# Optimization experiments

Measured on AMD Instinct MI355X. Metric: run time of the kernel, lower is better.

Reference implementation:

```python
import jax, jax.numpy as jnp
import numpy as np

B = 1024        # number of molecule pairs (batch_don.max()+1)
LMAX = 160      # static pad length per molecule (avg ~64 atoms, 12-sigma safe)
D = 128         # embed_dim
H = 4           # num_heads
HD = D // H     # head_dim
SCALE = HD ** -0.5
LN_EPS = 1e-5


def setup_inputs() -> dict:
    key = jax.random.key(0)
    ks = jax.random.split(key, 16)
    N = 65536
    x_don = jax.random.normal(ks[0], (N, D), jnp.float32)
    x_acc = jax.random.normal(ks[1], (N, D), jnp.float32)
    batch_don = jnp.sort(jax.random.randint(ks[2], (N,), 0, B)).astype(jnp.int32)
    batch_acc = jnp.sort(jax.random.randint(ks[3], (N,), 0, B)).astype(jnp.int32)
    s = 1.0 / np.sqrt(D)
    Wq = jax.random.uniform(ks[4], (D, D), jnp.float32, -s, s)
    bq = jax.random.uniform(ks[5], (D,), jnp.float32, -s, s)
    Wk = jax.random.uniform(ks[6], (D, D), jnp.float32, -s, s)
    bk = jax.random.uniform(ks[7], (D,), jnp.float32, -s, s)
    Wv = jax.random.uniform(ks[8], (D, D), jnp.float32, -s, s)
    bv = jax.random.uniform(ks[9], (D,), jnp.float32, -s, s)
    Wo = jax.random.uniform(ks[10], (D, D), jnp.float32, -s, s)
    bo = jax.random.uniform(ks[11], (D,), jnp.float32, -s, s)
    ln_g = jnp.ones((D,), jnp.float32)
    ln_b = jnp.zeros((D,), jnp.float32)
    return {"x_don": x_don, "x_acc": x_acc, "Wq": Wq, "bq": bq, "Wk": Wk, "bk": bk,
            "Wv": Wv, "bv": bv, "Wo": Wo, "bo": bo, "ln_g": ln_g, "ln_b": ln_b,
            "batch_don": batch_don, "batch_acc": batch_acc}


def _pad_segments(x, batch):
    # sorted segment ids -> padded [B, LMAX, D], valid mask [B, LMAX], per-row pos
    n = x.shape[0]
    counts = jnp.zeros((B,), jnp.int32).at[batch].add(1)
    starts = jnp.concatenate([jnp.zeros((1,), jnp.int32), jnp.cumsum(counts)[:-1]])
    pos = jnp.arange(n, dtype=jnp.int32) - starts[batch]
    padded = jnp.zeros((B, LMAX, x.shape[1]), x.dtype).at[batch, pos].set(x)
    mask = jnp.arange(LMAX, dtype=jnp.int32)[None, :] < counts[:, None]
    return padded, mask, pos


def _layer_norm(x, g, b):
    mu = jnp.mean(x, axis=-1, keepdims=True)
    var = jnp.mean((x - mu) ** 2, axis=-1, keepdims=True)
    return (x - mu) * jax.lax.rsqrt(var + LN_EPS) * g + b


def _cross_attn(q_pad, kv_pad, k_mask, Wq, bq, Wk, bk, Wv, bv, Wo, bo, ln_g, ln_b):
    # q_pad: [B, Lq, D], kv_pad: [B, Lk, D], k_mask: [B, Lk]
    Q = (q_pad @ Wq + bq).reshape(B, LMAX, H, HD)
    K = (kv_pad @ Wk + bk).reshape(B, LMAX, H, HD)
    V = (kv_pad @ Wv + bv).reshape(B, LMAX, H, HD)
    scores = jnp.einsum('bqhd,bkhd->bhqk', Q, K) * SCALE
    scores = jnp.where(k_mask[:, None, None, :], scores, -1e30)
    m = jnp.max(scores, axis=-1, keepdims=True)
    e = jnp.exp(scores - m) * k_mask[:, None, None, :]
    attn = e / jnp.maximum(jnp.sum(e, axis=-1, keepdims=True), 1e-9)
    attended = jnp.einsum('bhqk,bkhd->bqhd', attn, V).reshape(B, LMAX, D)
    attended = attended @ Wo + bo
    # NOTE: the original module uses self.norm_don for BOTH directions (norm_acc unused)
    return _layer_norm(q_pad + attended, ln_g, ln_b)


def reference(x_don, x_acc, Wq, bq, Wk, bk, Wv, bv, Wo, bo, ln_g, ln_b, batch_don, batch_acc):
    don_pad, don_mask, don_pos = _pad_segments(x_don, batch_don)
    acc_pad, acc_mask, acc_pos = _pad_segments(x_acc, batch_acc)
    out_don = _cross_attn(don_pad, acc_pad, acc_mask, Wq, bq, Wk, bk, Wv, bv, Wo, bo, ln_g, ln_b)
    out_acc = _cross_attn(acc_pad, don_pad, don_mask, Wq, bq, Wk, bk, Wv, bv, Wo, bo, ln_g, ln_b)
    x_don_enriched = out_don[batch_don, don_pos]
    x_acc_enriched = out_acc[batch_acc, acc_pos]
    return (x_don_enriched, x_acc_enriched)
```

## Files before the change

kernel.cpp:

```cpp
#include <hip/hip_runtime.h>
#include <stdint.h>

#define NB 1024
#define LMAX 160
#define DIM 128
#define NH 4
#define HDIM 32
#define ATT_SCALE 0.1767766952966369f
#define LN_EPS 1e-5f
#define VTP 164
#define PSP 40
#define WTP 136

typedef __attribute__((ext_vector_type(8))) short bf16x8;
typedef __attribute__((ext_vector_type(4))) float f32x4;

union U8 { uint2 u[2]; uint4 q; bf16x8 v; };

__device__ __forceinline__ ushort f2bf(float f) {
    uint32_t x = __float_as_uint(f);
    x += 0x7fffu + ((x >> 16) & 1u);
    return (ushort)(x >> 16);
}
__device__ __forceinline__ uint32_t pk2bf(float a, float b) {
    return (uint32_t)f2bf(a) | ((uint32_t)f2bf(b) << 16);
}

__device__ __forceinline__ void wgbar_noflush() {
    asm volatile("s_waitcnt lgkmcnt(0)" ::: "memory");
    __builtin_amdgcn_s_barrier();
    asm volatile("" ::: "memory");
}

__global__ void setup_kernel(const float* __restrict__ Wq, const float* __restrict__ Wk,
                             const float* __restrict__ Wv, const float* __restrict__ Wo,
                             ushort* __restrict__ wtg,
                             const int* __restrict__ bd, const int* __restrict__ ba,
                             int* __restrict__ starts, int* __restrict__ counts, int N)
{
    int t = blockIdx.x * blockDim.x + threadIdx.x;
    {
        int m = t >> 14;
        int idx = t & 16383;
        int k = idx >> 7, c = idx & 127;
        const float* W = (m == 0) ? Wq : (m == 1) ? Wk : (m == 2) ? Wv : Wo;
        wtg[(m << 14) + c * DIM + k] = f2bf(W[idx]);
    }
    if (t < 2 * NB) {
        int side = t >> 10;
        int b = t & (NB - 1);
        const int* arr = side ? ba : bd;
        int lo = 0, hi = N;
        while (lo < hi) { int mid = (lo + hi) >> 1; if (arr[mid] < b) lo = mid + 1; else hi = mid; }
        int st = lo;
        hi = N;
        while (lo < hi) { int mid = (lo + hi) >> 1; if (arr[mid] < b + 1) lo = mid + 1; else hi = mid; }
        starts[t] = st;
        counts[t] = lo - st;
    }
}

__global__ __launch_bounds__(256) void proj_mfma(
    const float* __restrict__ x_don, const float* __restrict__ x_acc,
    const ushort* __restrict__ wtg,
    const float* __restrict__ bq, const float* __restrict__ bk, const float* __restrict__ bv,
    ushort* __restrict__ qkv, int N)
{
    __shared__ ushort wt[128][WTP];
    const int side = blockIdx.y;
    const float* x = side ? x_acc : x_don;
    const int t = threadIdx.x;
    const int lane = t & 63, wid = t >> 6;
    const int r16 = lane & 15, kg = lane >> 4;
    const int wr0 = blockIdx.x * 128 + wid * 32;

    float4 raw[2][4][2];
    #pragma unroll
    for (int rt = 0; rt < 2; ++rt) {
        const float* xr = &x[(size_t)(wr0 + rt * 16 + r16) * DIM + kg * 8];
        #pragma unroll
        for (int ks = 0; ks < 4; ++ks) {
            raw[rt][ks][0] = *reinterpret_cast<const float4*>(xr + ks * 32);
            raw[rt][ks][1] = *reinterpret_cast<const float4*>(xr + ks * 32 + 4);
        }
    }
    U8 xb[2][4];
    #pragma unroll
    for (int rt = 0; rt < 2; ++rt)
        #pragma unroll
        for (int ks = 0; ks < 4; ++ks) {
            xb[rt][ks].u[0].x = pk2bf(raw[rt][ks][0].x, raw[rt][ks][0].y);
            xb[rt][ks].u[0].y = pk2bf(raw[rt][ks][0].z, raw[rt][ks][0].w);
            xb[rt][ks].u[1].x = pk2bf(raw[rt][ks][1].x, raw[rt][ks][1].y);
            xb[rt][ks].u[1].y = pk2bf(raw[rt][ks][1].z, raw[rt][ks][1].w);
        }

    for (int w = 0; w < 3; ++w) {
        if (w) wgbar_noflush();

        const ushort* wsrc = wtg + ((size_t)w << 14);
        #pragma unroll
        for (int p = 0; p < 8; ++p) {
            int lin = (p * 256 + t) * 8;
            int c = lin >> 7, k = lin & 127;
            *reinterpret_cast<uint4*>(&wt[c][k]) =
                *reinterpret_cast<const uint4*>(&wsrc[c * DIM + k]);
        }
        wgbar_noflush();

        f32x4 acc[2][8];
        #pragma unroll
        for (int i = 0; i < 2; ++i)
            #pragma unroll
            for (int j = 0; j < 8; ++j) acc[i][j] = (f32x4){0.f, 0.f, 0.f, 0.f};

        #pragma unroll
        for (int ks = 0; ks < 4; ++ks)
            #pragma unroll
            for (int ct = 0; ct < 8; ++ct) {
                bf16x8 bfr = *reinterpret_cast<const bf16x8*>(
                    &wt[ct * 16 + r16][ks * 32 + kg * 8]);
                acc[0][ct] = __builtin_amdgcn_mfma_f32_16x16x32_bf16(xb[0][ks].v, bfr, acc[0][ct], 0, 0, 0);
                acc[1][ct] = __builtin_amdgcn_mfma_f32_16x16x32_bf16(xb[1][ks].v, bfr, acc[1][ct], 0, 0, 0);
            }

        const float* bias = (w == 0) ? bq : (w == 1) ? bk : bv;
        float b8[8];
        #pragma unroll
        for (int ct = 0; ct < 8; ++ct) b8[ct] = bias[ct * 16 + r16];
        ushort* outp = qkv + (size_t)(side * 3 + w) * N * DIM;
        #pragma unroll
        for (int rt = 0; rt < 2; ++rt)
            #pragma unroll
            for (int ct = 0; ct < 8; ++ct)
                #pragma unroll
                for (int j = 0; j < 4; ++j) {
                    int rr = wr0 + rt * 16 + kg * 4 + j;
                    outp[(size_t)rr * DIM + ct * 16 + r16] = f2bf(acc[rt][ct][j] + b8[ct]);
                }
    }
}

__global__ __launch_bounds__(64, 4) void attn_mfma(
    ushort* __restrict__ qkv,
    const int* __restrict__ starts, const int* __restrict__ counts, int N)
{
    __shared__ __align__(16) ushort Vt[HDIM][VTP];
    __shared__ __align__(16) ushort Ps[16][PSP];
    const int b = blockIdx.x, dir = blockIdx.y;
    const int hcol = blockIdx.z * HDIM;
    const int qside = dir, kside = 1 - dir;
    const int qs = starts[qside * NB + b];
    const int nq = counts[qside * NB + b];
    if (nq == 0) return;
    const int kst = starts[kside * NB + b];
    const int nk = min(counts[kside * NB + b], LMAX);
    ushort* Q = qkv + (size_t)(qside * 3) * N * DIM;
    const ushort* K = qkv + (size_t)(kside * 3 + 1) * N * DIM;
    const ushort* V = qkv + (size_t)(kside * 3 + 2) * N * DIM;
    const int lane = threadIdx.x;
    const int r16 = lane & 15, g = lane >> 4;

    const int NCK = (nk + 31) >> 5;
    const int NKP = NCK << 5;

    {
        const int krl = lane >> 2, c = lane & 3;
        for (int base = 0; base < nk; base += 16) {
            int kr = base + krl;
            if (kr < nk) {
                uint4 v4 = *reinterpret_cast<const uint4*>(
                    &V[(size_t)(kst + kr) * DIM + hcol + c * 8]);
                uint32_t vv[4] = {v4.x, v4.y, v4.z, v4.w};
                #pragma unroll
                for (int m2 = 0; m2 < 4; ++m2) {
                    Vt[c * 8 + 2 * m2][kr]     = (ushort)(vv[m2] & 0xffffu);
                    Vt[c * 8 + 2 * m2 + 1][kr] = (ushort)(vv[m2] >> 16);
                }
            }
        }
        int pad = NKP - nk;
        for (int i = lane; i < (pad << 5); i += 64) {
            int d = i & 31, col = nk + (i >> 5);
            Vt[d][col] = 0;
        }
    }
    __syncthreads();

    for (int q0 = 0; q0 < nq; q0 += 16) {
        const int rq = qs + min(q0 + r16, nq - 1);
        bf16x8 bQ = *reinterpret_cast<const bf16x8*>(&Q[(size_t)rq * DIM + hcol + g * 8]);

        float m = -1e30f, l = 0.f;
        f32x4 oa0 = {0.f, 0.f, 0.f, 0.f}, oa1 = {0.f, 0.f, 0.f, 0.f};

        for (int ck = 0; ck < NCK; ++ck) {
            const int k0 = ck * 32;
            const int rk0 = kst + min(k0 + r16, nk - 1);
            const int rk1 = kst + min(k0 + 16 + r16, nk - 1);
            bf16x8 aK0 = *reinterpret_cast<const bf16x8*>(&K[(size_t)rk0 * DIM + hcol + g * 8]);
            bf16x8 aK1 = *reinterpret_cast<const bf16x8*>(&K[(size_t)rk1 * DIM + hcol + g * 8]);
            f32x4 s0 = __builtin_amdgcn_mfma_f32_16x16x32_bf16(
                aK0, bQ, (f32x4){0.f, 0.f, 0.f, 0.f}, 0, 0, 0);
            f32x4 s1 = __builtin_amdgcn_mfma_f32_16x16x32_bf16(
                aK1, bQ, (f32x4){0.f, 0.f, 0.f, 0.f}, 0, 0, 0);

            float sv[8];
            #pragma unroll
            for (int j = 0; j < 4; ++j) {
                sv[j]     = (k0 + 4 * g + j < nk)      ? s0[j] * ATT_SCALE : -1e30f;
                sv[4 + j] = (k0 + 16 + 4 * g + j < nk) ? s1[j] * ATT_SCALE : -1e30f;
            }
            float tm = fmaxf(fmaxf(fmaxf(sv[0], sv[1]), fmaxf(sv[2], sv[3])),
                             fmaxf(fmaxf(sv[4], sv[5]), fmaxf(sv[6], sv[7])));
            tm = fmaxf(tm, __shfl_xor(tm, 16));
            tm = fmaxf(tm, __shfl_xor(tm, 32));

            bool up = tm > m + 8.f;
            float mn = up ? tm : m;
            float corr = up ? __expf(m - tm) : 1.f;

            float e[8];
            #pragma unroll
            for (int j = 0; j < 8; ++j) e[j] = __expf(sv[j] - mn);
            float ps = ((e[0] + e[1]) + (e[2] + e[3])) + ((e[4] + e[5]) + (e[6] + e[7]));
            ps += __shfl_xor(ps, 16);
            ps += __shfl_xor(ps, 32);
            l = l * corr + ps;
            m = mn;
            #pragma unroll
            for (int j = 0; j < 4; ++j) { oa0[j] *= corr; oa1[j] *= corr; }

            uint2 w0, w1;
            w0.x = pk2bf(e[0], e[1]);
            w0.y = pk2bf(e[2], e[3]);
            w1.x = pk2bf(e[4], e[5]);
            w1.y = pk2bf(e[6], e[7]);
            *reinterpret_cast<uint2*>(&Ps[r16][4 * g]) = w0;
            *reinterpret_cast<uint2*>(&Ps[r16][16 + 4 * g]) = w1;
            bf16x8 bP = *reinterpret_cast<const bf16x8*>(&Ps[r16][g * 8]);

            U8 av0, av1;
            av0.u[0] = *reinterpret_cast<const uint2*>(&Vt[r16][k0 + g * 8]);
            av0.u[1] = *reinterpret_cast<const uint2*>(&Vt[r16][k0 + g * 8 + 4]);
            av1.u[0] = *reinterpret_cast<const uint2*>(&Vt[16 + r16][k0 + g * 8]);
            av1.u[1] = *reinterpret_cast<const uint2*>(&Vt[16 + r16][k0 + g * 8 + 4]);
            oa0 = __builtin_amdgcn_mfma_f32_16x16x32_bf16(av0.v, bP, oa0, 0, 0, 0);
            oa1 = __builtin_amdgcn_mfma_f32_16x16x32_bf16(av1.v, bP, oa1, 0, 0, 0);
        }

        if (q0 + r16 < nq) {
            float inv = 1.f / fmaxf(l, 1e-9f);
            ushort* dst = &Q[(size_t)(qs + q0 + r16) * DIM + hcol];
            uint2 o0, o1;
            o0.x = pk2bf(oa0[0] * inv, oa0[1] * inv);
            o0.y = pk2bf(oa0[2] * inv, oa0[3] * inv);
            o1.x = pk2bf(oa1[0] * inv, oa1[1] * inv);
            o1.y = pk2bf(oa1[2] * inv, oa1[3] * inv);
            *reinterpret_cast<uint2*>(dst + 4 * g) = o0;
            *reinterpret_cast<uint2*>(dst + 16 + 4 * g) = o1;
        }
    }
}

__global__ __launch_bounds__(256) void out_mfma(
    const ushort* __restrict__ qkv,
    const float* __restrict__ x_don, const float* __restrict__ x_acc,
    const ushort* __restrict__ wtg,
    const float* __restrict__ bo, const float* __restrict__ ln_g, const float* __restrict__ ln_b,
    float* __restrict__ out, int N)
{
    __shared__ ushort wt[128][WTP];
    const int t = threadIdx.x;
    const int lane = t & 63, wid = t >> 6;
    const int r16 = lane & 15, kg = lane >> 4;
    const int r0 = blockIdx.x * 128;
    const int wr0 = r0 + wid * 32;
    const ushort* attb = qkv + (r0 < N ? (size_t)0 : (size_t)2 * N * DIM);
    const float* xresb = (r0 < N) ? x_don : x_acc;
    const int rx0 = (r0 < N) ? wr0 : wr0 - N;

    const ushort* wsrc = wtg + ((size_t)3 << 14);
    #pragma unroll
    for (int p = 0; p < 8; ++p) {
        int lin = (p * 256 + t) * 8;
        int c = lin >> 7, k = lin & 127;
        *reinterpret_cast<uint4*>(&wt[c][k]) =
            *reinterpret_cast<const uint4*>(&wsrc[c * DIM + k]);
    }

    U8 ab[2][4];
    #pragma unroll
    for (int rt = 0; rt < 2; ++rt)
        #pragma unroll
        for (int ks = 0; ks < 4; ++ks)
            ab[rt][ks].q = *reinterpret_cast<const uint4*>(
                &attb[(size_t)(wr0 + rt * 16 + r16) * DIM + ks * 32 + kg * 8]);

    __syncthreads();

    f32x4 acc[2][8];
    #pragma unroll
    for (int i = 0; i < 2; ++i)
        #pragma unroll
        for (int j = 0; j < 8; ++j) acc[i][j] = (f32x4){0.f, 0.f, 0.f, 0.f};

    #pragma unroll
    for (int ks = 0; ks < 4; ++ks)
        #pragma unroll
        for (int ct = 0; ct < 8; ++ct) {
            bf16x8 bfr = *reinterpret_cast<const bf16x8*>(
                &wt[ct * 16 + r16][ks * 32 + kg * 8]);
            acc[0][ct] = __builtin_amdgcn_mfma_f32_16x16x32_bf16(ab[0][ks].v, bfr, acc[0][ct], 0, 0, 0);
            acc[1][ct] = __builtin_amdgcn_mfma_f32_16x16x32_bf16(ab[1][ks].v, bfr, acc[1][ct], 0, 0, 0);
        }

    float bo8[8], g8[8], be8[8];
    #pragma unroll
    for (int ct = 0; ct < 8; ++ct) {
        int c = ct * 16 + r16;
        bo8[ct] = bo[c]; g8[ct] = ln_g[c]; be8[ct] = ln_b[c];
    }

    #pragma unroll
    for (int rt = 0; rt < 2; ++rt) {
        #pragma unroll
        for (int j = 0; j < 4; ++j) {
            int rl = rt * 16 + kg * 4 + j;
            const float* resr = &xresb[(size_t)(rx0 + rl) * DIM];
            float y[8];
            float s = 0.f, ss = 0.f;
            #pragma unroll
            for (int ct = 0; ct < 8; ++ct) {
                float v = acc[rt][ct][j] + bo8[ct] + resr[ct * 16 + r16];
                y[ct] = v; s += v; ss += v * v;
            }
            #pragma unroll
            for (int mk2 = 1; mk2 < 16; mk2 <<= 1) {
                s  += __shfl_xor(s, mk2);
                ss += __shfl_xor(ss, mk2);
            }
            float mu   = s * (1.f / 128.f);
            float var  = ss * (1.f / 128.f) - mu * mu;
            float rinv = rsqrtf(var + LN_EPS);
            #pragma unroll
            for (int ct = 0; ct < 8; ++ct)
                out[(size_t)(wr0 + rl) * DIM + ct * 16 + r16] =
                    (y[ct] - mu) * rinv * g8[ct] + be8[ct];
        }
    }
}

extern "C" void kernel_launch(void* const* d_in, const int* in_sizes, int n_in,
                              void* d_out, int out_size, void* d_ws, size_t ws_size,
                              hipStream_t stream)
{
    const float* x_don = (const float*)d_in[0];
    const float* x_acc = (const float*)d_in[1];
    const float* Wq = (const float*)d_in[2];  const float* bq = (const float*)d_in[3];
    const float* Wk = (const float*)d_in[4];  const float* bk = (const float*)d_in[5];
    const float* Wv = (const float*)d_in[6];  const float* bv = (const float*)d_in[7];
    const float* Wo = (const float*)d_in[8];  const float* bo = (const float*)d_in[9];
    const float* ln_g = (const float*)d_in[10]; const float* ln_b = (const float*)d_in[11];
    const int* batch_don = (const int*)d_in[12];
    const int* batch_acc = (const int*)d_in[13];
    const int N = in_sizes[0] / DIM;
    float* out = (float*)d_out;

    char* ws = (char*)d_ws;
    int* starts = (int*)ws;
    int* counts = starts + 2 * NB;
    ushort* qkv = (ushort*)(ws + 16384);
    ushort* wtg = (ushort*)(ws + 16384 + (size_t)6 * N * DIM * 2);

    setup_kernel<<<256, 256, 0, stream>>>(Wq, Wk, Wv, Wo, wtg,
                                          batch_don, batch_acc, starts, counts, N);

    dim3 gproj(N / 128, 2);
    proj_mfma<<<gproj, 256, 0, stream>>>(x_don, x_acc, wtg, bq, bk, bv, qkv, N);

    dim3 gattn(NB, 2, NH);
    attn_mfma<<<gattn, 64, 0, stream>>>(qkv, starts, counts, N);

    out_mfma<<<(2 * N) / 128, 256, 0, stream>>>(qkv, x_don, x_acc, wtg,
                                                bo, ln_g, ln_b, out, N);
}
```

Measured before the change: 138.0 us.

## Fuse Q projection into attention kernel, drop Q from projection pass

The projection kernel now computes only K and V. Each attention block instead reads the fp32 query rows, converts them to bf16 and multiplies them with its head's 32-column slice of Wq using MFMA. The result is staged through a small LDS tile and fed straight into the score computation. This removes the Q write and re-read through global memory and one third of the projection work, but every query row's fp32 data is now re-read once per head (four times) and the tiny GEMM runs inside the latency-bound attention loop.

```diff
diff --git a/kernel.cpp b/kernel.cpp
--- a/kernel.cpp
+++ b/kernel.cpp
@@ -63,7 +63,7 @@
 __global__ __launch_bounds__(256) void proj_mfma(
     const float* __restrict__ x_don, const float* __restrict__ x_acc,
     const ushort* __restrict__ wtg,
-    const float* __restrict__ bq, const float* __restrict__ bk, const float* __restrict__ bv,
+    const float* __restrict__ bk, const float* __restrict__ bv,
     ushort* __restrict__ qkv, int N)
 {
     __shared__ ushort wt[128][WTP];
@@ -95,9 +95,8 @@
             xb[rt][ks].u[1].y = pk2bf(raw[rt][ks][1].z, raw[rt][ks][1].w);
         }
 
-    for (int w = 0; w < 3; ++w) {
-        if (w) wgbar_noflush();
-
+    for (int w = 1; w < 3; ++w) {
+        if (w > 1) wgbar_noflush();
         const ushort* wsrc = wtg + ((size_t)w << 14);
         #pragma unroll
         for (int p = 0; p < 8; ++p) {
@@ -124,7 +123,7 @@
                 acc[1][ct] = __builtin_amdgcn_mfma_f32_16x16x32_bf16(xb[1][ks].v, bfr, acc[1][ct], 0, 0, 0);
             }
 
-        const float* bias = (w == 0) ? bq : (w == 1) ? bk : bv;
+        const float* bias = (w == 1) ? bk : bv;
         float b8[8];
         #pragma unroll
         for (int ct = 0; ct < 8; ++ct) b8[ct] = bias[ct * 16 + r16];
@@ -143,10 +142,13 @@
 
 __global__ __launch_bounds__(64, 4) void attn_mfma(
     ushort* __restrict__ qkv,
+    const float* __restrict__ x_don, const float* __restrict__ x_acc,
+    const ushort* __restrict__ wtg, const float* __restrict__ bq,
     const int* __restrict__ starts, const int* __restrict__ counts, int N)
 {
     __shared__ __align__(16) ushort Vt[HDIM][VTP];
     __shared__ __align__(16) ushort Ps[16][PSP];
+    __shared__ __align__(16) ushort Qt[16][PSP];
     const int b = blockIdx.x, dir = blockIdx.y;
     const int hcol = blockIdx.z * HDIM;
     const int qside = dir, kside = 1 - dir;
@@ -158,6 +160,7 @@
     ushort* Q = qkv + (size_t)(qside * 3) * N * DIM;
     const ushort* K = qkv + (size_t)(kside * 3 + 1) * N * DIM;
     const ushort* V = qkv + (size_t)(kside * 3 + 2) * N * DIM;
+    const float* xq = qside ? x_acc : x_don;
     const int lane = threadIdx.x;
     const int r16 = lane & 15, g = lane >> 4;
 
@@ -187,9 +190,47 @@
     }
     __syncthreads();
 
+    bf16x8 wbq[2][4];
+    #pragma unroll
+    for (int ct = 0; ct < 2; ++ct)
+        #pragma unroll
+        for (int ks = 0; ks < 4; ++ks)
+            wbq[ct][ks] = *reinterpret_cast<const bf16x8*>(
+                &wtg[(hcol + ct * 16 + r16) * DIM + ks * 32 + g * 8]);
+    const float bq0 = bq[hcol + r16];
+    const float bq1 = bq[hcol + 16 + r16];
+
     for (int q0 = 0; q0 < nq; q0 += 16) {
-        const int rq = qs + min(q0 + r16, nq - 1);
-        bf16x8 bQ = *reinterpret_cast<const bf16x8*>(&Q[(size_t)rq * DIM + hcol + g * 8]);
+        {
+            int rowc = qs + min(q0 + r16, nq - 1);
+            const float* xr = &xq[(size_t)rowc * DIM + g * 8];
+            float4 raw[4][2];
+            #pragma unroll
+            for (int ks = 0; ks < 4; ++ks) {
+                raw[ks][0] = *reinterpret_cast<const float4*>(xr + ks * 32);
+                raw[ks][1] = *reinterpret_cast<const float4*>(xr + ks * 32 + 4);
+            }
+            U8 xb[4];
+            #pragma unroll
+            for (int ks = 0; ks < 4; ++ks) {
+                xb[ks].u[0].x = pk2bf(raw[ks][0].x, raw[ks][0].y);
+                xb[ks].u[0].y = pk2bf(raw[ks][0].z, raw[ks][0].w);
+                xb[ks].u[1].x = pk2bf(raw[ks][1].x, raw[ks][1].y);
+                xb[ks].u[1].y = pk2bf(raw[ks][1].z, raw[ks][1].w);
+            }
+            f32x4 a0 = {0.f, 0.f, 0.f, 0.f}, a1 = {0.f, 0.f, 0.f, 0.f};
+            #pragma unroll
+            for (int ks = 0; ks < 4; ++ks) {
+                a0 = __builtin_amdgcn_mfma_f32_16x16x32_bf16(xb[ks].v, wbq[0][ks], a0, 0, 0, 0);
+                a1 = __builtin_amdgcn_mfma_f32_16x16x32_bf16(xb[ks].v, wbq[1][ks], a1, 0, 0, 0);
+            }
+            #pragma unroll
+            for (int j = 0; j < 4; ++j) {
+                Qt[g * 4 + j][r16]      = f2bf(a0[j] + bq0);
+                Qt[g * 4 + j][16 + r16] = f2bf(a1[j] + bq1);
+            }
+        }
+        bf16x8 bQ = *reinterpret_cast<const bf16x8*>(&Qt[r16][g * 8]);
 
         float m = -1e30f, l = 0.f;
         f32x4 oa0 = {0.f, 0.f, 0.f, 0.f}, oa1 = {0.f, 0.f, 0.f, 0.f};
@@ -377,10 +418,11 @@
                                           batch_don, batch_acc, starts, counts, N);
 
     dim3 gproj(N / 128, 2);
-    proj_mfma<<<gproj, 256, 0, stream>>>(x_don, x_acc, wtg, bq, bk, bv, qkv, N);
+    proj_mfma<<<gproj, 256, 0, stream>>>(x_don, x_acc, wtg, bk, bv, qkv, N);
 
     dim3 gattn(NB, 2, NH);
-    attn_mfma<<<gattn, 64, 0, stream>>>(qkv, starts, counts, N);
+    attn_mfma<<<gattn, 64, 0, stream>>>(qkv, x_don, x_acc, wtg, bq,
+                                        starts, counts, N);
 
     out_mfma<<<(2 * N) / 128, 256, 0, stream>>>(qkv, x_don, x_acc, wtg,
                                                 bo, ln_g, ln_b, out, N);
```

New measurement: 164.8 us. +19.4%, slower.
